# Optimization experiments

Measured on AMD Instinct MI355X. Metric: run time of the kernel, lower is better.

Reference implementation:

```python
import jax, jax.numpy as jnp
import numpy as np

# Sampled-subgraph sizes (NeighborSampler layout): N0 sources -> N1 -> B seeds
N0, N1, B = 500_000, 100_000, 10_000
E0, E1 = 1_000_000, 100_000
F_IN, HID, C = 128, 256, 40
TEMP = 1.0  # cfg.temparature, dot-product attention kernel in Summarize


def sage_layer(x_src, x_tgt, src, dst, n_tgt, Wl, b, Wr):
    """PyG SAGEConv (mean aggr): lin_l(mean_{j in N(i)} x_j) + lin_r(x_i)."""
    msg = x_src[src]                                              # [E, d] gather
    s = jax.ops.segment_sum(msg, dst, num_segments=n_tgt)        # [n_tgt, d]
    cnt = jax.ops.segment_sum(jnp.ones((src.shape[0],), x_src.dtype), dst,
                              num_segments=n_tgt)
    agg = s / jnp.maximum(cnt, 1.0)[:, None]
    return agg @ Wl + b + x_tgt @ Wr


def setup_inputs() -> dict:
    key = jax.random.key(0)
    ks = jax.random.split(key, 12)
    return {
        "x": jax.random.normal(ks[0], (N0, F_IN), jnp.float32),
        "src0": jax.random.randint(ks[1], (E0,), 0, N0, dtype=jnp.int32),
        "dst0": jax.random.randint(ks[2], (E0,), 0, N1, dtype=jnp.int32),
        "src1": jax.random.randint(ks[3], (E1,), 0, N1, dtype=jnp.int32),
        "dst1": jax.random.randint(ks[4], (E1,), 0, B, dtype=jnp.int32),
        "W1l": jax.random.normal(ks[5], (F_IN, HID), jnp.float32) / np.float32(np.sqrt(F_IN)),
        "b1": jnp.zeros((HID,), jnp.float32),
        "W1r": jax.random.normal(ks[6], (F_IN, HID), jnp.float32) / np.float32(np.sqrt(F_IN)),
        "W2l": jax.random.normal(ks[7], (HID, HID), jnp.float32) / np.float32(np.sqrt(HID)),
        "b2": jnp.zeros((HID,), jnp.float32),
        "W2r": jax.random.normal(ks[8], (HID, HID), jnp.float32) / np.float32(np.sqrt(HID)),
        "Wout": jax.random.normal(ks[9], (HID, C), jnp.float32) / np.float32(np.sqrt(HID)),
        "bout": jnp.zeros((C,), jnp.float32),
        "batch_size": B,
    }


def reference(x, src0, dst0, src1, dst1, W1l, b1, W1r, W2l, b2, W2r, Wout, bout, batch_size):
    # twin branch starts as detached copy of seed-node features
    x_ = x[:batch_size]
    # --- layer 1 (dropout omitted: eval mode) ---
    h = jax.nn.relu(sage_layer(x, x[:N1], src0, dst0, N1, W1l, b1, W1r))   # [N1, HID]
    h_ = jax.nn.relu(x_ @ W1r)                                             # twin: root-weight only
    hs = [h[:batch_size]]
    hs_ = [h_]
    # --- layer 2 ---
    h2 = jax.nn.relu(sage_layer(h, h[:batch_size], src1, dst1, batch_size, W2l, b2, W2r))  # [B, HID]
    h2_ = jax.nn.relu(h_ @ W2r)
    hs.append(h2)
    hs_.append(h2_)
    # --- Summarize: dot-kernel attention over layer representations ---
    Hs = jnp.stack(hs, axis=1)    # [B, L, HID]
    Qs = jnp.stack(hs_, axis=1)   # [B, L, HID] twin queries
    scores = jnp.sum(Hs * Qs, axis=-1) / TEMP          # [B, L]
    alpha = jax.nn.softmax(scores, axis=1)
    h_out = jnp.sum(alpha[..., None] * Hs, axis=1)     # [B, HID]
    return h_out @ Wout + bout                          # [B, C]
```

## Files before the change

kernel.cpp:

```cpp
#include <hip/hip_runtime.h>
#include <cstddef>


namespace {

constexpr int N1i  = 100000;
constexpr int Bni  = 10000;
constexpr int E0i  = 1000000;
constexpr int E1i  = 100000;
constexpr int FIN  = 128;
constexpr int HID  = 256;
constexpr int NCLS = 40;

typedef __attribute__((ext_vector_type(8))) short short8;
typedef __attribute__((ext_vector_type(8))) unsigned short ushort8;
typedef __attribute__((ext_vector_type(4))) unsigned short us4;
typedef __attribute__((ext_vector_type(4))) float floatx4;


__global__ void hist_both_kernel(const int* __restrict__ dst0, const int* __restrict__ dst1,
                                 int* __restrict__ cnt0, int* __restrict__ cnt1) {
    int i = blockIdx.x * blockDim.x + threadIdx.x;
    if (i < E0i) atomicAdd(&cnt0[dst0[i]], 1);
    else if (i < E0i + E1i) atomicAdd(&cnt1[dst1[i - E0i]], 1);
}

__global__ void partial_sum_both_kernel(const int* __restrict__ cnt0, const int* __restrict__ cnt1,
                                        int* __restrict__ bsum0, int* __restrict__ bsum1, int nb0) {
    __shared__ int s[256];
    const int* cnt; int n; int* bsum; int bi;
    if ((int)blockIdx.x < nb0) { cnt = cnt0; n = N1i; bsum = bsum0; bi = blockIdx.x; }
    else                       { cnt = cnt1; n = Bni; bsum = bsum1; bi = blockIdx.x - nb0; }
    int i = bi * 256 + threadIdx.x;
    s[threadIdx.x] = (i < n) ? cnt[i] : 0;
    __syncthreads();
    for (int o = 128; o > 0; o >>= 1) {
        if (threadIdx.x < o) s[threadIdx.x] += s[threadIdx.x + o];
        __syncthreads();
    }
    if (threadIdx.x == 0) bsum[bi] = s[0];
}

__global__ void scan_bsum_both_kernel(int* __restrict__ bsum0, int nb0, int* __restrict__ tot0,
                                      int* __restrict__ bsum1, int nb1, int* __restrict__ tot1) {
    __shared__ int s[512];
    int* bsum; int nb; int* tot;
    if (blockIdx.x == 0) { bsum = bsum0; nb = nb0; tot = tot0; }
    else                 { bsum = bsum1; nb = nb1; tot = tot1; }
    int t = threadIdx.x;
    int v = (t < nb) ? bsum[t] : 0;
    s[t] = v;
    __syncthreads();
    for (int o = 1; o < 512; o <<= 1) {
        int u = (t >= o) ? s[t - o] : 0;
        __syncthreads();
        s[t] += u;
        __syncthreads();
    }
    if (t < nb) bsum[t] = s[t] - v;
    if (t == 511) *tot = s[511];
}

__global__ void scan_final_both_kernel(int* __restrict__ cnt0, const int* __restrict__ bsum0, int* __restrict__ rp0,
                                       int* __restrict__ cnt1, const int* __restrict__ bsum1, int* __restrict__ rp1,
                                       int nb0) {
    __shared__ int s[256];
    int* cnt; const int* bsum; int* rp; int n; int bi;
    if ((int)blockIdx.x < nb0) { cnt = cnt0; bsum = bsum0; rp = rp0; n = N1i; bi = blockIdx.x; }
    else                       { cnt = cnt1; bsum = bsum1; rp = rp1; n = Bni; bi = blockIdx.x - nb0; }
    int t = threadIdx.x;
    int i = bi * 256 + t;
    int v = (i < n) ? cnt[i] : 0;
    s[t] = v;
    __syncthreads();
    for (int o = 1; o < 256; o <<= 1) {
        int u = (t >= o) ? s[t - o] : 0;
        __syncthreads();
        s[t] += u;
        __syncthreads();
    }
    if (i < n) {
        int r = bsum[bi] + s[t] - v;
        rp[i]  = r;
        cnt[i] = r;
    }
}

__global__ void scatter_both_kernel(const int* __restrict__ src0, const int* __restrict__ dst0,
                                    const int* __restrict__ src1, const int* __restrict__ dst1,
                                    int* __restrict__ cur0, int* __restrict__ cur1,
                                    int* __restrict__ es0, int* __restrict__ es1) {
    int i = blockIdx.x * blockDim.x + threadIdx.x;
    if (i < E0i) {
        int p = atomicAdd(&cur0[dst0[i]], 1);
        es0[p] = src0[i];
    } else if (i < E0i + E1i) {
        int j = i - E0i;
        int p = atomicAdd(&cur1[dst1[j]], 1);
        es1[p] = src1[j];
    }
}


__device__ inline unsigned short bf16_rne_u(unsigned u) {
    unsigned r = u + 0x7fffu + ((u >> 16) & 1u);
    return (unsigned short)(r >> 16);
}

__device__ inline void split1(float f, unsigned short& hs, unsigned short& ls) {
    hs = bf16_rne_u(__float_as_uint(f));
    float lo = f - __uint_as_float((unsigned)hs << 16);
    ls = bf16_rne_u(__float_as_uint(lo));
}


__global__ __launch_bounds__(256) void agg_mean128_kernel(
    const float* __restrict__ x, const int* __restrict__ rp,
    const int* __restrict__ es,
    unsigned short* __restrict__ aggh, unsigned short* __restrict__ aggl, int ntgt) {
    int tgt  = blockIdx.x * 4 + (threadIdx.x >> 6);
    int lane = threadIdx.x & 63;
    if (tgt >= ntgt) return;
    int b = rp[tgt], e = rp[tgt + 1];
    int d = e - b;
    int half = lane >> 5;
    int sl   = lane & 31;
    float4 acc = {0.f, 0.f, 0.f, 0.f};
    const float* xp = x + sl * 4;
    for (int base = 0; base < d; base += 64) {
        int rem = d - base; if (rem > 64) rem = 64;
        int li  = lane < rem ? lane : rem - 1;
        int idx = es[b + base + li];
        int rm1 = rem - 1;
        int npair = (rem + 1) >> 1;
        for (int p = 0; p < npair; p += 8) {
            int e0 = p * 2 + half;
            int s0 = e0      <= rm1 ? e0      : rm1;
            int s1 = e0 + 2  <= rm1 ? e0 + 2  : rm1;
            int s2 = e0 + 4  <= rm1 ? e0 + 4  : rm1;
            int s3 = e0 + 6  <= rm1 ? e0 + 6  : rm1;
            int s4 = e0 + 8  <= rm1 ? e0 + 8  : rm1;
            int s5 = e0 + 10 <= rm1 ? e0 + 10 : rm1;
            int s6 = e0 + 12 <= rm1 ? e0 + 12 : rm1;
            int s7 = e0 + 14 <= rm1 ? e0 + 14 : rm1;
            float w0 = (e0      < rem) ? 1.f : 0.f;
            float w1 = (e0 + 2  < rem) ? 1.f : 0.f;
            float w2 = (e0 + 4  < rem) ? 1.f : 0.f;
            float w3 = (e0 + 6  < rem) ? 1.f : 0.f;
            float w4 = (e0 + 8  < rem) ? 1.f : 0.f;
            float w5 = (e0 + 10 < rem) ? 1.f : 0.f;
            float w6 = (e0 + 12 < rem) ? 1.f : 0.f;
            float w7 = (e0 + 14 < rem) ? 1.f : 0.f;
            int i0 = __shfl(idx, s0), i1 = __shfl(idx, s1);
            int i2 = __shfl(idx, s2), i3 = __shfl(idx, s3);
            int i4 = __shfl(idx, s4), i5 = __shfl(idx, s5);
            int i6 = __shfl(idx, s6), i7 = __shfl(idx, s7);
            float4 v0 = *(const float4*)(xp + i0 * FIN);
            float4 v1 = *(const float4*)(xp + i1 * FIN);
            float4 v2 = *(const float4*)(xp + i2 * FIN);
            float4 v3 = *(const float4*)(xp + i3 * FIN);
            float4 v4 = *(const float4*)(xp + i4 * FIN);
            float4 v5 = *(const float4*)(xp + i5 * FIN);
            float4 v6 = *(const float4*)(xp + i6 * FIN);
            float4 v7 = *(const float4*)(xp + i7 * FIN);
            acc.x += v0.x * w0 + v1.x * w1 + v2.x * w2 + v3.x * w3
                   + v4.x * w4 + v5.x * w5 + v6.x * w6 + v7.x * w7;
            acc.y += v0.y * w0 + v1.y * w1 + v2.y * w2 + v3.y * w3
                   + v4.y * w4 + v5.y * w5 + v6.y * w6 + v7.y * w7;
            acc.z += v0.z * w0 + v1.z * w1 + v2.z * w2 + v3.z * w3
                   + v4.z * w4 + v5.z * w5 + v6.z * w6 + v7.z * w7;
            acc.w += v0.w * w0 + v1.w * w1 + v2.w * w2 + v3.w * w3
                   + v4.w * w4 + v5.w * w5 + v6.w * w6 + v7.w * w7;
        }
    }
    acc.x += __shfl_xor(acc.x, 32);
    acc.y += __shfl_xor(acc.y, 32);
    acc.z += __shfl_xor(acc.z, 32);
    acc.w += __shfl_xor(acc.w, 32);
    if (lane < 32) {
        float inv = 1.0f / fmaxf((float)d, 1.0f);
        float f[4] = {acc.x * inv, acc.y * inv, acc.z * inv, acc.w * inv};
        us4 hv, lv;
#pragma unroll
        for (int j = 0; j < 4; j++) { unsigned short hs, ls; split1(f[j], hs, ls); hv[j] = hs; lv[j] = ls; }
        *(us4*)(aggh + (size_t)tgt * FIN + sl * 4) = hv;
        *(us4*)(aggl + (size_t)tgt * FIN + sl * 4) = lv;
    }
}

__global__ __launch_bounds__(256) void agg_mean256_kernel(
    const float* __restrict__ h, const int* __restrict__ rp,
    const int* __restrict__ es,
    unsigned short* __restrict__ aggh, unsigned short* __restrict__ aggl, int ntgt) {
    int tgt  = blockIdx.x * 4 + (threadIdx.x >> 6);
    int lane = threadIdx.x & 63;
    if (tgt >= ntgt) return;
    int b = rp[tgt], e = rp[tgt + 1];
    int d = e - b;
    float4 acc = {0.f, 0.f, 0.f, 0.f};
    const float* hp = h + lane * 4;
    for (int base = 0; base < d; base += 64) {
        int rem = d - base; if (rem > 64) rem = 64;
        int li  = lane < rem ? lane : rem - 1;
        int idx = es[b + base + li];
        int rm1 = rem - 1;
        for (int j = 0; j < rem; j += 8) {
            int s0 = j     <= rm1 ? j     : rm1;
            int s1 = j + 1 <= rm1 ? j + 1 : rm1;
            int s2 = j + 2 <= rm1 ? j + 2 : rm1;
            int s3 = j + 3 <= rm1 ? j + 3 : rm1;
            int s4 = j + 4 <= rm1 ? j + 4 : rm1;
            int s5 = j + 5 <= rm1 ? j + 5 : rm1;
            int s6 = j + 6 <= rm1 ? j + 6 : rm1;
            int s7 = j + 7 <= rm1 ? j + 7 : rm1;
            float w0 = 1.f;
            float w1 = (j + 1 < rem) ? 1.f : 0.f;
            float w2 = (j + 2 < rem) ? 1.f : 0.f;
            float w3 = (j + 3 < rem) ? 1.f : 0.f;
            float w4 = (j + 4 < rem) ? 1.f : 0.f;
            float w5 = (j + 5 < rem) ? 1.f : 0.f;
            float w6 = (j + 6 < rem) ? 1.f : 0.f;
            float w7 = (j + 7 < rem) ? 1.f : 0.f;
            int i0 = __shfl(idx, s0), i1 = __shfl(idx, s1);
            int i2 = __shfl(idx, s2), i3 = __shfl(idx, s3);
            int i4 = __shfl(idx, s4), i5 = __shfl(idx, s5);
            int i6 = __shfl(idx, s6), i7 = __shfl(idx, s7);
            float4 v0 = *(const float4*)(hp + i0 * HID);
            float4 v1 = *(const float4*)(hp + i1 * HID);
            float4 v2 = *(const float4*)(hp + i2 * HID);
            float4 v3 = *(const float4*)(hp + i3 * HID);
            float4 v4 = *(const float4*)(hp + i4 * HID);
            float4 v5 = *(const float4*)(hp + i5 * HID);
            float4 v6 = *(const float4*)(hp + i6 * HID);
            float4 v7 = *(const float4*)(hp + i7 * HID);
            acc.x += v0.x * w0 + v1.x * w1 + v2.x * w2 + v3.x * w3
                   + v4.x * w4 + v5.x * w5 + v6.x * w6 + v7.x * w7;
            acc.y += v0.y * w0 + v1.y * w1 + v2.y * w2 + v3.y * w3
                   + v4.y * w4 + v5.y * w5 + v6.y * w6 + v7.y * w7;
            acc.z += v0.z * w0 + v1.z * w1 + v2.z * w2 + v3.z * w3
                   + v4.z * w4 + v5.z * w5 + v6.z * w6 + v7.z * w7;
            acc.w += v0.w * w0 + v1.w * w1 + v2.w * w2 + v3.w * w3
                   + v4.w * w4 + v5.w * w5 + v6.w * w6 + v7.w * w7;
        }
    }
    float inv = 1.0f / fmaxf((float)d, 1.0f);
    float f[4] = {acc.x * inv, acc.y * inv, acc.z * inv, acc.w * inv};
    us4 hv, lv;
#pragma unroll
    for (int j = 0; j < 4; j++) { unsigned short hs, ls; split1(f[j], hs, ls); hv[j] = hs; lv[j] = ls; }
    *(us4*)(aggh + (size_t)tgt * HID + lane * 4) = hv;
    *(us4*)(aggl + (size_t)tgt * HID + lane * 4) = lv;
}


__global__ void wtrans_all_kernel(const float* __restrict__ W1l, const float* __restrict__ W1r,
                                  const float* __restrict__ W2l, const float* __restrict__ W2r,
                                  unsigned short* __restrict__ w1lh, unsigned short* __restrict__ w1ll,
                                  unsigned short* __restrict__ w1rh, unsigned short* __restrict__ w1rl,
                                  unsigned short* __restrict__ w2lh, unsigned short* __restrict__ w2ll,
                                  unsigned short* __restrict__ w2rh, unsigned short* __restrict__ w2rl) {
    int e = blockIdx.x * 256 + threadIdx.x;
    const float* W; unsigned short* hiT; unsigned short* loT; int K; int idx;
    if (e < 65536) {
        K = 128;
        if (e < 32768) { W = W1l; hiT = w1lh; loT = w1ll; idx = e; }
        else           { W = W1r; hiT = w1rh; loT = w1rl; idx = e - 32768; }
    } else {
        K = 256;
        int e2 = e - 65536;
        if (e2 < 65536) { W = W2l; hiT = w2lh; loT = w2ll; idx = e2; }
        else            { W = W2r; hiT = w2rh; loT = w2rl; idx = e2 - 65536; }
    }
    int k = idx >> 8, n = idx & 255;
    unsigned short hs, ls;
    split1(W[idx], hs, ls);
    hiT[n * K + k] = hs;
    loT[n * K + k] = ls;
}


__device__ inline void cvt_store8(unsigned short* hi_dst, unsigned short* lo_dst,
                                  const float* v) {
    ushort8 hv, lv;
#pragma unroll
    for (int i = 0; i < 8; i++) {
        unsigned short hs, ls;
        split1(v[i], hs, ls);
        hv[i] = hs;
        lv[i] = ls;
    }
    *(ushort8*)hi_dst = hv;
    *(ushort8*)lo_dst = lv;
}

__global__ __launch_bounds__(512, 2) void gemm_dual_kernel(
    const unsigned short* __restrict__ A1ha, const unsigned short* __restrict__ A1la,
    const float* __restrict__ A2a,
    const unsigned short* __restrict__ B1ha, const unsigned short* __restrict__ B1la,
    const unsigned short* __restrict__ B2ha, const unsigned short* __restrict__ B2la,
    const float* __restrict__ biasa, float* __restrict__ Ca, int Ma, int K1a, int K2a, int nmba,
    const float* __restrict__ A1fb,
    const unsigned short* __restrict__ B1hb, const unsigned short* __restrict__ B1lb,
    float* __restrict__ Cb, int Mb, int K1b) {
    constexpr int LDAS = 40;
    __shared__ __align__(16) unsigned short Ah[128 * LDAS];
    __shared__ __align__(16) unsigned short Al[128 * LDAS];
    __shared__ __align__(16) unsigned short Bh[256 * LDAS];
    __shared__ __align__(16) unsigned short Bl[256 * LDAS];

    const unsigned short *A1h, *A1l;
    const float *A1f, *A2;
    const unsigned short *B1h, *B1l, *B2h, *B2l;
    const float* bias; float* C; int M, K1, K2;
    bool jobA;
    int mb = blockIdx.x;
    if (mb < nmba) {
        jobA = true;
        A1h = A1ha; A1l = A1la; A1f = nullptr; A2 = A2a;
        B1h = B1ha; B1l = B1la; B2h = B2ha; B2l = B2la;
        bias = biasa; C = Ca; M = Ma; K1 = K1a; K2 = K2a;
    } else {
        jobA = false;
        mb -= nmba;
        A1h = nullptr; A1l = nullptr; A1f = A1fb; A2 = nullptr;
        B1h = B1hb; B1l = B1lb; B2h = nullptr; B2l = nullptr;
        bias = nullptr; C = Cb; M = Mb; K1 = K1b; K2 = 0;
    }
    const int Kt = K1 + K2;
    const int m0 = mb * 128;

    const int tid  = threadIdx.x;
    const int lane = tid & 63;
    const int wave = tid >> 6;
    const int wm   = (wave & 1) * 64;
    const int wn   = (wave >> 1) * 64;
    const int arow_l = tid >> 2;
    const int acol   = (tid & 3) * 8;
    const int brow   = tid >> 1;
    const int bcol   = (tid & 1) * 16;
    const int frow = lane & 15;
    const int fk   = (lane >> 4) * 8;

    int arow = m0 + arow_l; if (arow >= M) arow = M - 1;

    floatx4 acc[4][4] = {};

    float4 pa0, pa1;
    ushort8 pah, pal;
    ushort8 ph0, ph1, pl0, pl1;
    if (jobA) {
        pah = *(const ushort8*)(A1h + (size_t)arow * K1 + acol);
        pal = *(const ushort8*)(A1l + (size_t)arow * K1 + acol);
    } else {
        const float* ap = A1f + (size_t)arow * K1 + acol;
        pa0 = *(const float4*)(ap);
        pa1 = *(const float4*)(ap + 4);
    }
    {
        const unsigned short* bhp = B1h + (size_t)brow * K1 + bcol;
        const unsigned short* blp = B1l + (size_t)brow * K1 + bcol;
        ph0 = *(const ushort8*)bhp;       ph1 = *(const ushort8*)(bhp + 8);
        pl0 = *(const ushort8*)blp;       pl1 = *(const ushort8*)(blp + 8);
    }

    for (int k0 = 0; k0 < Kt; k0 += 32) {
        bool splitPhase = jobA && (k0 < K1);
        __syncthreads();
        if (splitPhase) {
            *(ushort8*)&Ah[arow_l * LDAS + acol] = pah;
            *(ushort8*)&Al[arow_l * LDAS + acol] = pal;
        } else {
            float av[8] = {pa0.x, pa0.y, pa0.z, pa0.w, pa1.x, pa1.y, pa1.z, pa1.w};
            cvt_store8(&Ah[arow_l * LDAS + acol], &Al[arow_l * LDAS + acol], av);
        }
        *(ushort8*)&Bh[brow * LDAS + bcol]     = ph0;
        *(ushort8*)&Bh[brow * LDAS + bcol + 8] = ph1;
        *(ushort8*)&Bl[brow * LDAS + bcol]     = pl0;
        *(ushort8*)&Bl[brow * LDAS + bcol + 8] = pl1;
        __syncthreads();
        if (k0 + 32 < Kt) {
            int kn = k0 + 32;
            if (kn < K1) {
                if (jobA) {
                    pah = *(const ushort8*)(A1h + (size_t)arow * K1 + kn + acol);
                    pal = *(const ushort8*)(A1l + (size_t)arow * K1 + kn + acol);
                } else {
                    const float* ap = A1f + (size_t)arow * K1 + kn + acol;
                    pa0 = *(const float4*)(ap);
                    pa1 = *(const float4*)(ap + 4);
                }
                const unsigned short* bhp = B1h + (size_t)brow * K1 + kn + bcol;
                const unsigned short* blp = B1l + (size_t)brow * K1 + kn + bcol;
                ph0 = *(const ushort8*)bhp;   ph1 = *(const ushort8*)(bhp + 8);
                pl0 = *(const ushort8*)blp;   pl1 = *(const ushort8*)(blp + 8);
            } else {
                int kk = kn - K1;
                const float* ap = A2 + (size_t)arow * K2 + kk + acol;
                pa0 = *(const float4*)(ap);
                pa1 = *(const float4*)(ap + 4);
                const unsigned short* bhp = B2h + (size_t)brow * K2 + kk + bcol;
                const unsigned short* blp = B2l + (size_t)brow * K2 + kk + bcol;
                ph0 = *(const ushort8*)bhp;   ph1 = *(const ushort8*)(bhp + 8);
                pl0 = *(const ushort8*)blp;   pl1 = *(const ushort8*)(blp + 8);
            }
        }

        short8 ahf[4], alf[4], bhf[4], blf[4];
#pragma unroll
        for (int t = 0; t < 4; t++) {
            int ar = (wm + t * 16 + frow) * LDAS + fk;
            ahf[t] = *(const short8*)&Ah[ar];
            alf[t] = *(const short8*)&Al[ar];
            int br = (wn + t * 16 + frow) * LDAS + fk;
            bhf[t] = *(const short8*)&Bh[br];
            blf[t] = *(const short8*)&Bl[br];
        }
#pragma unroll
        for (int i = 0; i < 4; i++) {
#pragma unroll
            for (int j = 0; j < 4; j++) {
                acc[i][j] = __builtin_amdgcn_mfma_f32_16x16x32_bf16(ahf[i], bhf[j], acc[i][j], 0, 0, 0);
                acc[i][j] = __builtin_amdgcn_mfma_f32_16x16x32_bf16(ahf[i], blf[j], acc[i][j], 0, 0, 0);
                acc[i][j] = __builtin_amdgcn_mfma_f32_16x16x32_bf16(alf[i], bhf[j], acc[i][j], 0, 0, 0);
            }
        }
    }

    const int colL = lane & 15;
    const int quad = lane >> 4;
#pragma unroll
    for (int j = 0; j < 4; j++) {
        int c = wn + j * 16 + colL;
        float bj = bias ? bias[c] : 0.0f;
#pragma unroll
        for (int i = 0; i < 4; i++) {
            int rbase = m0 + wm + i * 16 + quad * 4;
#pragma unroll
            for (int r = 0; r < 4; r++) {
                int row = rbase + r;
                if (row < M) {
                    float v = acc[i][j][r] + bj;
                    v = fmaxf(v, 0.0f);
                    C[(size_t)row * 256 + c] = v;
                }
            }
        }
    }
}


__global__ __launch_bounds__(256) void attn_out_kernel(
    const float* __restrict__ h, const float* __restrict__ h2,
    const float* __restrict__ q1, const float* __restrict__ q2,
    const float* __restrict__ Wout, const float* __restrict__ bout,
    float* __restrict__ out, int Bn) {
    int w = threadIdx.x >> 6, lane = threadIdx.x & 63;
    int row = blockIdx.x * 4 + w;
    __shared__ __align__(16) float cbuf[4][260];
    if (row < Bn) {
        const float4 a = *(const float4*)(h  + (size_t)row * HID + lane * 4);
        const float4 p = *(const float4*)(q1 + (size_t)row * HID + lane * 4);
        const float4 b = *(const float4*)(h2 + (size_t)row * HID + lane * 4);
        const float4 q = *(const float4*)(q2 + (size_t)row * HID + lane * 4);
        float s0 = a.x * p.x + a.y * p.y + a.z * p.z + a.w * p.w;
        float s1 = b.x * q.x + b.y * q.y + b.z * q.z + b.w * q.w;
        for (int o = 32; o > 0; o >>= 1) {
            s0 += __shfl_xor(s0, o);
            s1 += __shfl_xor(s1, o);
        }
        float m  = fmaxf(s0, s1);
        float e0 = __expf(s0 - m), e1 = __expf(s1 - m);
        float inv = 1.0f / (e0 + e1);
        float a0 = e0 * inv, a1 = e1 * inv;
        float4 cv;
        cv.x = a0 * a.x + a1 * b.x; cv.y = a0 * a.y + a1 * b.y;
        cv.z = a0 * a.z + a1 * b.z; cv.w = a0 * a.w + a1 * b.w;
        *(float4*)&cbuf[w][lane * 4] = cv;
    }
    __syncthreads();
    int t = threadIdx.x;
    if (t < 4 * NCLS) {
        int r = t / NCLS, j = t % NCLS;
        int orow = blockIdx.x * 4 + r;
        if (orow < Bn) {
            float acc = bout[j];
#pragma unroll 8
            for (int k = 0; k < HID; k++) acc += cbuf[r][k] * Wout[k * NCLS + j];
            out[(size_t)orow * NCLS + j] = acc;
        }
    }
}

}

extern "C" void kernel_launch(void* const* d_in, const int* in_sizes, int n_in,
                              void* d_out, int out_size, void* d_ws, size_t ws_size,
                              hipStream_t stream) {
    const float* x    = (const float*)d_in[0];
    const int*   src0 = (const int*)d_in[1];
    const int*   dst0 = (const int*)d_in[2];
    const int*   src1 = (const int*)d_in[3];
    const int*   dst1 = (const int*)d_in[4];
    const float* W1l  = (const float*)d_in[5];
    const float* b1   = (const float*)d_in[6];
    const float* W1r  = (const float*)d_in[7];
    const float* W2l  = (const float*)d_in[8];
    const float* b2   = (const float*)d_in[9];
    const float* W2r  = (const float*)d_in[10];
    const float* Wout = (const float*)d_in[11];
    const float* bout = (const float*)d_in[12];
    float* out = (float*)d_out;

    char* ws = (char*)d_ws;
    size_t off = 0;
    auto alloc = [&](size_t bytes) {
        void* p = ws + off;
        off = (off + bytes + 255) & ~(size_t)255;
        return p;
    };
    int* cnt0  = (int*)alloc((size_t)(N1i + Bni) * sizeof(int));
    int* cnt1  = cnt0 + N1i;
    int* rp0   = (int*)alloc((N1i + 1) * sizeof(int));
    int* rp1   = (int*)alloc((Bni + 1) * sizeof(int));
    int* bsum0 = (int*)alloc(512 * sizeof(int));
    int* bsum1 = (int*)alloc(512 * sizeof(int));
    int* es0   = (int*)alloc(E0i * sizeof(int));
    int* es1   = (int*)alloc(E1i * sizeof(int));
    unsigned short* w1l_hi = (unsigned short*)alloc(256 * FIN * sizeof(unsigned short));
    unsigned short* w1l_lo = (unsigned short*)alloc(256 * FIN * sizeof(unsigned short));
    unsigned short* w1r_hi = (unsigned short*)alloc(256 * FIN * sizeof(unsigned short));
    unsigned short* w1r_lo = (unsigned short*)alloc(256 * FIN * sizeof(unsigned short));
    unsigned short* w2l_hi = (unsigned short*)alloc(256 * HID * sizeof(unsigned short));
    unsigned short* w2l_lo = (unsigned short*)alloc(256 * HID * sizeof(unsigned short));
    unsigned short* w2r_hi = (unsigned short*)alloc(256 * HID * sizeof(unsigned short));
    unsigned short* w2r_lo = (unsigned short*)alloc(256 * HID * sizeof(unsigned short));
    unsigned short* agg0h = (unsigned short*)alloc((size_t)N1i * FIN * sizeof(unsigned short));
    unsigned short* agg0l = (unsigned short*)alloc((size_t)N1i * FIN * sizeof(unsigned short));
    unsigned short* agg1h = (unsigned short*)alloc((size_t)Bni * HID * sizeof(unsigned short));
    unsigned short* agg1l = (unsigned short*)alloc((size_t)Bni * HID * sizeof(unsigned short));
    float* h   = (float*)alloc((size_t)N1i * HID * sizeof(float));
    float* hq1 = (float*)alloc((size_t)Bni * HID * sizeof(float));
    float* h2  = (float*)alloc((size_t)Bni * HID * sizeof(float));
    float* h2q = (float*)alloc((size_t)Bni * HID * sizeof(float));

    const int nb0 = (N1i + 255) / 256, nb1 = (Bni + 255) / 256;
    const int nmb1g = (N1i + 127) / 128;
    const int nmbB  = (Bni + 127) / 128;

    hipMemsetAsync(cnt0, 0, (size_t)(N1i + Bni) * sizeof(int), stream);
    wtrans_all_kernel<<<768, 256, 0, stream>>>(W1l, W1r, W2l, W2r,
        w1l_hi, w1l_lo, w1r_hi, w1r_lo, w2l_hi, w2l_lo, w2r_hi, w2r_lo);
    hist_both_kernel<<<(E0i + E1i + 255) / 256, 256, 0, stream>>>(dst0, dst1, cnt0, cnt1);
    partial_sum_both_kernel<<<nb0 + nb1, 256, 0, stream>>>(cnt0, cnt1, bsum0, bsum1, nb0);
    scan_bsum_both_kernel<<<2, 512, 0, stream>>>(bsum0, nb0, rp0 + N1i, bsum1, nb1, rp1 + Bni);
    scan_final_both_kernel<<<nb0 + nb1, 256, 0, stream>>>(cnt0, bsum0, rp0, cnt1, bsum1, rp1, nb0);
    scatter_both_kernel<<<(E0i + E1i + 255) / 256, 256, 0, stream>>>(
        src0, dst0, src1, dst1, cnt0, cnt1, es0, es1);

    agg_mean128_kernel<<<(N1i + 3) / 4, 256, 0, stream>>>(x, rp0, es0, agg0h, agg0l, N1i);
    gemm_dual_kernel<<<nmb1g + nmbB, 512, 0, stream>>>(
        agg0h, agg0l, x, w1l_hi, w1l_lo, w1r_hi, w1r_lo, b1, h, N1i, 128, 128, nmb1g,
        x, w1r_hi, w1r_lo, hq1, Bni, 128);

    agg_mean256_kernel<<<(Bni + 3) / 4, 256, 0, stream>>>(h, rp1, es1, agg1h, agg1l, Bni);
    gemm_dual_kernel<<<nmbB + nmbB, 512, 0, stream>>>(
        agg1h, agg1l, h, w2l_hi, w2l_lo, w2r_hi, w2r_lo, b2, h2, Bni, 256, 256, nmbB,
        hq1, w2r_hi, w2r_lo, h2q, Bni, 256);

    attn_out_kernel<<<(Bni + 3) / 4, 256, 0, stream>>>(h, h2, hq1, h2q, Wout, bout, out, Bni);
}
```

Before: 728.6 us.

## Compute layer-1 outputs only for nodes consumed by layer 2

```diff
diff --git a/kernel.cpp b/kernel.cpp
--- a/kernel.cpp
+++ b/kernel.cpp
@@ -19,18 +19,32 @@
 
 
 __global__ void hist_both_kernel(const int* __restrict__ dst0, const int* __restrict__ dst1,
-                                 int* __restrict__ cnt0, int* __restrict__ cnt1) {
+                                 const int* __restrict__ src1,
+                                 int* __restrict__ cnt0, int* __restrict__ cnt1,
+                                 int* __restrict__ mask,
+                                 int* __restrict__ ilist, int* __restrict__ icnt) {
     int i = blockIdx.x * blockDim.x + threadIdx.x;
     if (i < E0i) atomicAdd(&cnt0[dst0[i]], 1);
     else if (i < E0i + E1i) atomicAdd(&cnt1[dst1[i - E0i]], 1);
+    else if (i < E0i + 2 * E1i) mask[src1[i - E0i - E1i]] = 1;
+    else if (i < E0i + 2 * E1i + Bni) {
+        int j = i - E0i - 2 * E1i;
+        mask[j] = 1;
+        ilist[j] = j;
+        if (j == 0) *icnt = Bni;
+    }
 }
 
 __global__ void partial_sum_both_kernel(const int* __restrict__ cnt0, const int* __restrict__ cnt1,
-                                        int* __restrict__ bsum0, int* __restrict__ bsum1, int nb0) {
+                                        const int* __restrict__ mask,
+                                        int* __restrict__ bsum0, int* __restrict__ bsum1,
+                                        int* __restrict__ bsum2, int nb0, int nb1) {
     __shared__ int s[256];
     const int* cnt; int n; int* bsum; int bi;
-    if ((int)blockIdx.x < nb0) { cnt = cnt0; n = N1i; bsum = bsum0; bi = blockIdx.x; }
-    else                       { cnt = cnt1; n = Bni; bsum = bsum1; bi = blockIdx.x - nb0; }
+    int bx = blockIdx.x;
+    if (bx < nb0)            { cnt = cnt0; n = N1i; bsum = bsum0; bi = bx; }
+    else if (bx < nb0 + nb1) { cnt = cnt1; n = Bni; bsum = bsum1; bi = bx - nb0; }
+    else                     { cnt = mask; n = N1i; bsum = bsum2; bi = bx - nb0 - nb1; }
     int i = bi * 256 + threadIdx.x;
     s[threadIdx.x] = (i < n) ? cnt[i] : 0;
     __syncthreads();
@@ -42,11 +56,13 @@
 }
 
 __global__ void scan_bsum_both_kernel(int* __restrict__ bsum0, int nb0, int* __restrict__ tot0,
-                                      int* __restrict__ bsum1, int nb1, int* __restrict__ tot1) {
+                                      int* __restrict__ bsum1, int nb1, int* __restrict__ tot1,
+                                      int* __restrict__ bsum2, int* __restrict__ tot2) {
     __shared__ int s[512];
     int* bsum; int nb; int* tot;
-    if (blockIdx.x == 0) { bsum = bsum0; nb = nb0; tot = tot0; }
-    else                 { bsum = bsum1; nb = nb1; tot = tot1; }
+    if (blockIdx.x == 0)      { bsum = bsum0; nb = nb0; tot = tot0; }
+    else if (blockIdx.x == 1) { bsum = bsum1; nb = nb1; tot = tot1; }
+    else                      { bsum = bsum2; nb = nb0; tot = tot2; }
     int t = threadIdx.x;
     int v = (t < nb) ? bsum[t] : 0;
     s[t] = v;
@@ -63,11 +79,14 @@
 
 __global__ void scan_final_both_kernel(int* __restrict__ cnt0, const int* __restrict__ bsum0, int* __restrict__ rp0,
                                        int* __restrict__ cnt1, const int* __restrict__ bsum1, int* __restrict__ rp1,
-                                       int nb0) {
+                                       const int* __restrict__ mask, const int* __restrict__ bsum2,
+                                       int* __restrict__ list, int nb0, int nb1) {
     __shared__ int s[256];
-    int* cnt; const int* bsum; int* rp; int n; int bi;
-    if ((int)blockIdx.x < nb0) { cnt = cnt0; bsum = bsum0; rp = rp0; n = N1i; bi = blockIdx.x; }
-    else                       { cnt = cnt1; bsum = bsum1; rp = rp1; n = Bni; bi = blockIdx.x - nb0; }
+    const int* cnt; const int* bsum; int n; int bi; int job;
+    int bx = blockIdx.x;
+    if (bx < nb0)            { job = 0; cnt = cnt0; bsum = bsum0; n = N1i; bi = bx; }
+    else if (bx < nb0 + nb1) { job = 1; cnt = cnt1; bsum = bsum1; n = Bni; bi = bx - nb0; }
+    else                     { job = 2; cnt = mask; bsum = bsum2; n = N1i; bi = bx - nb0 - nb1; }
     int t = threadIdx.x;
     int i = bi * 256 + t;
     int v = (i < n) ? cnt[i] : 0;
@@ -81,8 +100,13 @@
     }
     if (i < n) {
         int r = bsum[bi] + s[t] - v;
-        rp[i]  = r;
-        cnt[i] = r;
+        if (job == 2) {
+            if (v) list[r] = i;
+        } else if (job == 0) {
+            rp0[i] = r; cnt0[i] = r;
+        } else {
+            rp1[i] = r; cnt1[i] = r;
+        }
     }
 }
 
@@ -116,12 +140,14 @@
 
 __global__ __launch_bounds__(256) void agg_mean128_kernel(
     const float* __restrict__ x, const int* __restrict__ rp,
-    const int* __restrict__ es,
-    unsigned short* __restrict__ aggh, unsigned short* __restrict__ aggl, int ntgt) {
-    int tgt  = blockIdx.x * 4 + (threadIdx.x >> 6);
+    const int* __restrict__ es, const int* __restrict__ list,
+    const int* __restrict__ nlistp,
+    unsigned short* __restrict__ aggh, unsigned short* __restrict__ aggl) {
+    int slot = blockIdx.x * 4 + (threadIdx.x >> 6);
+    if (slot >= *nlistp) return;
+    int node = list[slot];
     int lane = threadIdx.x & 63;
-    if (tgt >= ntgt) return;
-    int b = rp[tgt], e = rp[tgt + 1];
+    int b = rp[node], e = rp[node + 1];
     int d = e - b;
     int half = lane >> 5;
     int sl   = lane & 31;
@@ -183,8 +209,8 @@
         us4 hv, lv;
 #pragma unroll
         for (int j = 0; j < 4; j++) { unsigned short hs, ls; split1(f[j], hs, ls); hv[j] = hs; lv[j] = ls; }
-        *(us4*)(aggh + (size_t)tgt * FIN + sl * 4) = hv;
-        *(us4*)(aggl + (size_t)tgt * FIN + sl * 4) = lv;
+        *(us4*)(aggh + (size_t)slot * FIN + sl * 4) = hv;
+        *(us4*)(aggl + (size_t)slot * FIN + sl * 4) = lv;
     }
 }
 
@@ -298,7 +324,9 @@
     const float* __restrict__ A2a,
     const unsigned short* __restrict__ B1ha, const unsigned short* __restrict__ B1la,
     const unsigned short* __restrict__ B2ha, const unsigned short* __restrict__ B2la,
-    const float* __restrict__ biasa, float* __restrict__ Ca, int Ma, int K1a, int K2a, int nmba,
+    const float* __restrict__ biasa, float* __restrict__ Ca,
+    const int* __restrict__ list, const int* __restrict__ nlistp,
+    int K1a, int K2a, int nmba,
     const float* __restrict__ A1fb,
     const unsigned short* __restrict__ B1hb, const unsigned short* __restrict__ B1lb,
     float* __restrict__ Cb, int Mb, int K1b) {
@@ -307,24 +335,28 @@
     __shared__ __align__(16) unsigned short Al[128 * LDAS];
     __shared__ __align__(16) unsigned short Bh[256 * LDAS];
     __shared__ __align__(16) unsigned short Bl[256 * LDAS];
+    __shared__ int lsd[128];
 
     const unsigned short *A1h, *A1l;
     const float *A1f, *A2;
     const unsigned short *B1h, *B1l, *B2h, *B2l;
-    const float* bias; float* C; int M, K1, K2;
+    const float* bias; float* C; int K1, K2, M;
     bool jobA;
     int mb = blockIdx.x;
     if (mb < nmba) {
         jobA = true;
+        M = *nlistp;
+        if (mb * 128 >= M) return;
         A1h = A1ha; A1l = A1la; A1f = nullptr; A2 = A2a;
         B1h = B1ha; B1l = B1la; B2h = B2ha; B2l = B2la;
-        bias = biasa; C = Ca; M = Ma; K1 = K1a; K2 = K2a;
+        bias = biasa; C = Ca; K1 = K1a; K2 = K2a;
     } else {
         jobA = false;
         mb -= nmba;
+        M = Mb;
         A1h = nullptr; A1l = nullptr; A1f = A1fb; A2 = nullptr;
         B1h = B1hb; B1l = B1lb; B2h = nullptr; B2l = nullptr;
-        bias = nullptr; C = Cb; M = Mb; K1 = K1b; K2 = 0;
+        bias = nullptr; C = Cb; K1 = K1b; K2 = 0;
     }
     const int Kt = K1 + K2;
     const int m0 = mb * 128;
@@ -342,6 +374,12 @@
     const int fk   = (lane >> 4) * 8;
 
     int arow = m0 + arow_l; if (arow >= M) arow = M - 1;
+    const int arl = arow - m0;
+
+    if (jobA && tid < 128) {
+        int s = m0 + tid;
+        lsd[tid] = list[s < M ? s : M - 1];
+    }
 
     floatx4 acc[4][4] = {};
 
@@ -395,7 +433,8 @@
                 pl0 = *(const ushort8*)blp;   pl1 = *(const ushort8*)(blp + 8);
             } else {
                 int kk = kn - K1;
-                const float* ap = A2 + (size_t)arow * K2 + kk + acol;
+                int anode = lsd[arl];
+                const float* ap = A2 + (size_t)anode * K2 + kk + acol;
                 pa0 = *(const float4*)(ap);
                 pa1 = *(const float4*)(ap + 4);
                 const unsigned short* bhp = B2h + (size_t)brow * K2 + kk + bcol;
@@ -441,7 +480,8 @@
                 if (row < M) {
                     float v = acc[i][j][r] + bj;
                     v = fmaxf(v, 0.0f);
-                    C[(size_t)row * 256 + c] = v;
+                    size_t crow = jobA ? (size_t)lsd[row - m0] : (size_t)row;
+                    C[crow * 256 + c] = v;
                 }
             }
         }
@@ -518,12 +558,18 @@
         off = (off + bytes + 255) & ~(size_t)255;
         return p;
     };
-    int* cnt0  = (int*)alloc((size_t)(N1i + Bni) * sizeof(int));
+    int* cnt0  = (int*)alloc((size_t)(N1i + Bni + N1i) * sizeof(int));
     int* cnt1  = cnt0 + N1i;
+    int* mask  = cnt0 + N1i + Bni;
     int* rp0   = (int*)alloc((N1i + 1) * sizeof(int));
     int* rp1   = (int*)alloc((Bni + 1) * sizeof(int));
     int* bsum0 = (int*)alloc(512 * sizeof(int));
     int* bsum1 = (int*)alloc(512 * sizeof(int));
+    int* bsum2 = (int*)alloc(512 * sizeof(int));
+    int* list  = (int*)alloc((size_t)N1i * sizeof(int));
+    int* ilist = (int*)alloc((size_t)Bni * sizeof(int));
+    int* nlist = (int*)alloc(256);
+    int* icnt  = (int*)alloc(256);
     int* es0   = (int*)alloc(E0i * sizeof(int));
     int* es1   = (int*)alloc(E1i * sizeof(int));
     unsigned short* w1l_hi = (unsigned short*)alloc(256 * FIN * sizeof(unsigned short));
@@ -547,24 +593,31 @@
     const int nmb1g = (N1i + 127) / 128;
     const int nmbB  = (Bni + 127) / 128;
 
-    hipMemsetAsync(cnt0, 0, (size_t)(N1i + Bni) * sizeof(int), stream);
+    hipMemsetAsync(cnt0, 0, (size_t)(N1i + Bni + N1i) * sizeof(int), stream);
     wtrans_all_kernel<<<768, 256, 0, stream>>>(W1l, W1r, W2l, W2r,
         w1l_hi, w1l_lo, w1r_hi, w1r_lo, w2l_hi, w2l_lo, w2r_hi, w2r_lo);
-    hist_both_kernel<<<(E0i + E1i + 255) / 256, 256, 0, stream>>>(dst0, dst1, cnt0, cnt1);
-    partial_sum_both_kernel<<<nb0 + nb1, 256, 0, stream>>>(cnt0, cnt1, bsum0, bsum1, nb0);
-    scan_bsum_both_kernel<<<2, 512, 0, stream>>>(bsum0, nb0, rp0 + N1i, bsum1, nb1, rp1 + Bni);
-    scan_final_both_kernel<<<nb0 + nb1, 256, 0, stream>>>(cnt0, bsum0, rp0, cnt1, bsum1, rp1, nb0);
+    hist_both_kernel<<<(E0i + 2 * E1i + Bni + 255) / 256, 256, 0, stream>>>(
+        dst0, dst1, src1, cnt0, cnt1, mask, ilist, icnt);
+    partial_sum_both_kernel<<<nb0 + nb1 + nb0, 256, 0, stream>>>(
+        cnt0, cnt1, mask, bsum0, bsum1, bsum2, nb0, nb1);
+    scan_bsum_both_kernel<<<3, 512, 0, stream>>>(
+        bsum0, nb0, rp0 + N1i, bsum1, nb1, rp1 + Bni, bsum2, nlist);
+    scan_final_both_kernel<<<nb0 + nb1 + nb0, 256, 0, stream>>>(
+        cnt0, bsum0, rp0, cnt1, bsum1, rp1, mask, bsum2, list, nb0, nb1);
     scatter_both_kernel<<<(E0i + E1i + 255) / 256, 256, 0, stream>>>(
         src0, dst0, src1, dst1, cnt0, cnt1, es0, es1);
 
-    agg_mean128_kernel<<<(N1i + 3) / 4, 256, 0, stream>>>(x, rp0, es0, agg0h, agg0l, N1i);
+    agg_mean128_kernel<<<(N1i + 3) / 4, 256, 0, stream>>>(
+        x, rp0, es0, list, nlist, agg0h, agg0l);
     gemm_dual_kernel<<<nmb1g + nmbB, 512, 0, stream>>>(
-        agg0h, agg0l, x, w1l_hi, w1l_lo, w1r_hi, w1r_lo, b1, h, N1i, 128, 128, nmb1g,
+        agg0h, agg0l, x, w1l_hi, w1l_lo, w1r_hi, w1r_lo, b1, h, list, nlist,
+        128, 128, nmb1g,
         x, w1r_hi, w1r_lo, hq1, Bni, 128);
 
     agg_mean256_kernel<<<(Bni + 3) / 4, 256, 0, stream>>>(h, rp1, es1, agg1h, agg1l, Bni);
     gemm_dual_kernel<<<nmbB + nmbB, 512, 0, stream>>>(
-        agg1h, agg1l, h, w2l_hi, w2l_lo, w2r_hi, w2r_lo, b2, h2, Bni, 256, 256, nmbB,
+        agg1h, agg1l, h, w2l_hi, w2l_lo, w2r_hi, w2r_lo, b2, h2, ilist, icnt,
+        256, 256, nmbB,
         hq1, w2r_hi, w2r_lo, h2q, Bni, 256);
 
     attn_out_kernel<<<(Bni + 3) / 4, 256, 0, stream>>>(h, h2, hq1, h2q, Wout, bout, out, Bni);
```

New measurement: 675.2 us. 1.08x faster.
